# Kernel tuning notes

Hardware: AMD Instinct MI355X
Metric: run time of the kernel (lower is better)

## Reference

```python
import jax, jax.numpy as jnp
import numpy as np

N, B, D = 4, 256, 128  # agents, batch, latent dim; hidden = 2*D


def setup_inputs() -> dict:
    key = jax.random.key(0)
    k1, k2, k3, k4, k5 = jax.random.split(key, 5)
    z_all = jax.random.normal(k1, (N, B, D), dtype=jnp.float32)
    # per-agent MLP params, stacked over agents; torch Linear layout [out, in]
    W1 = jax.random.normal(k2, (N, 2 * D, D), dtype=jnp.float32) * 0.08
    b1 = jax.random.normal(k3, (N, 2 * D), dtype=jnp.float32) * 0.05
    W2 = jax.random.normal(k4, (N, 1, 2 * D), dtype=jnp.float32) * 0.06
    b2 = jax.random.normal(k5, (N, 1), dtype=jnp.float32) * 0.05
    return {"z_all": z_all, "W1": W1, "b1": b1, "W2": W2, "b2": b2}


def _value(z, W1i, b1i, W2i, b2i):
    # V_i(z): Linear(D,2D) -> tanh -> Linear(2D,1), squeezed to scalar
    h = jnp.tanh(W1i @ z + b1i)          # [2D]
    return jnp.dot(W2i[0], h) + b2i[0]   # scalar


def _pair_hessian(zb, W1i, b1i, W2i, b2i):
    # Hessian of V_i w.r.t. z, batched over B -> [B, D, D]
    hess = jax.hessian(lambda z: _value(z, W1i, b1i, W2i, b2i))
    return jax.vmap(hess)(zb)


def reference(z_all, W1, b1, W2, b2):
    Bn, Dn = z_all.shape[1], z_all.shape[2]
    zero = jnp.zeros((Bn, Dn, Dn), dtype=z_all.dtype)
    rows = []
    for i in range(N):
        cols = []
        for j in range(N):
            if i == j:
                cols.append(zero)
            else:
                cols.append(_pair_hessian(z_all[j], W1[i], b1[i], W2[i], b2[i]))
        rows.append(jnp.stack(cols, axis=0))
    return jnp.stack(rows, axis=0)  # [N, N, B, D, D]
```

## Files before the change

### kernel.cpp

```cpp
#include <hip/hip_runtime.h>
#include <hip/hip_bf16.h>

#define NA 4
#define BB 256
#define DDm 128
#define KKm 256

typedef __attribute__((ext_vector_type(4))) float f32x4;
typedef __attribute__((ext_vector_type(4))) unsigned int u32x4;
typedef __attribute__((ext_vector_type(8))) short bf16x8;

__device__ __forceinline__ unsigned int f2bf(float f) {
  unsigned int bits = __builtin_bit_cast(unsigned int, f);
  unsigned int lsb = (bits >> 16) & 1u;
  return (bits + 0x7fffu + lsb) >> 16;
}

__device__ __forceinline__ int swz_off(int a, int k2bytes) {
  return ((a << 9) + k2bytes) ^ ((a & 7) << 4);
}

__global__ __launch_bounds__(256) void prep_kernel(const float* __restrict__ W1,
                                                   unsigned short* __restrict__ Wt_g,
                                                   float* __restrict__ W1T) {
  int blk = blockIdx.x;
  int i = blk >> 3;
  int chunk = blk & 7;
  const float* W1i = W1 + i * KKm * DDm;
  char* Wti = (char*)(Wt_g + i * 32768);
  float* W1Ti = W1T + i * DDm * KKm;
  int base = chunk * 4096;
  for (int idx = base + threadIdx.x; idx < base + 4096; idx += 256) {
    int a = idx >> 8;
    int k = idx & 255;
    float v = W1i[k * DDm + a];
    W1Ti[a * KKm + k] = v;
    *(unsigned short*)(Wti + swz_off(a, k << 1)) = (unsigned short)f2bf(v);
  }
}

__global__ __launch_bounds__(256, 2) void hess_kernel(
    const float* __restrict__ z_all, const float* __restrict__ b1,
    const float* __restrict__ W2, const unsigned short* __restrict__ Wt_g,
    const float* __restrict__ W1T, float* __restrict__ out) {
  __shared__ __align__(16) unsigned short Wt[32768];
  __shared__ __align__(16) float s_lds[2][KKm];

  int t = threadIdx.x;
  int blk = blockIdx.x;
  int pair = blk >> 7;
  int bgrp = blk & 127;
  int i = pair >> 2;
  int j = pair & 3;

  if (i == j) {
    f32x4* zp = (f32x4*)(out + (((size_t)pair * BB + bgrp * 2) << 14));
    f32x4 z4 = (f32x4){0.f, 0.f, 0.f, 0.f};
#pragma unroll
    for (int q = 0; q < 32; ++q) zp[q * 256 + t] = z4;
    return;
  }

  {
    int wvi = t >> 6, lane = t & 63;
    const char* src = (const char*)(Wt_g + i * 32768);
#pragma unroll
    for (int it = 0; it < 16; ++it) {
      int off = (it * 4 + wvi) * 1024;
      __builtin_amdgcn_global_load_lds(
          (const __attribute__((address_space(1))) unsigned int*)(src + off + lane * 16),
          (__attribute__((address_space(3))) unsigned int*)((char*)Wt + off),
          16, 0, 0);
    }
  }

  {
    const float* w = W1T + i * DDm * KKm + t;
    const float* zj = z_all + ((size_t)j * BB + bgrp * 2) * DDm;
    float u0 = b1[i * KKm + t];
    float u1 = u0;
#pragma unroll 8
    for (int a = 0; a < DDm; ++a) {
      float wa = w[a * KKm];
      u0 = fmaf(wa, zj[a], u0);
      u1 = fmaf(wa, zj[DDm + a], u1);
    }
    float w2v = W2[i * KKm + t];
    float h0 = tanhf(u0), h1 = tanhf(u1);
    s_lds[0][t] = -2.0f * w2v * h0 * (1.0f - h0 * h0);
    s_lds[1][t] = -2.0f * w2v * h1 * (1.0f - h1 * h1);
  }
  __syncthreads();

  int wvi = t >> 6, lane = t & 63;
  int bl = wvi >> 1;
  int m0 = (wvi & 1) * 64;
  int g = lane >> 4;
  int lr = lane & 15;

  f32x4 acc[4][8];
#pragma unroll
  for (int mt = 0; mt < 4; ++mt)
#pragma unroll
    for (int nt = 0; nt < 8; ++nt) acc[mt][nt] = (f32x4){0.f, 0.f, 0.f, 0.f};

  for (int kc = 0; kc < 8; ++kc) {
    int kbyte = kc * 64 + g * 16;
    const f32x4* sp = (const f32x4*)&s_lds[bl][kc * 32 + g * 8];
    f32x4 sA = sp[0], sB = sp[1];
    float sv[8] = {sA[0], sA[1], sA[2], sA[3], sB[0], sB[1], sB[2], sB[3]};

    bf16x8 afr[4];
#pragma unroll
    for (int mt = 0; mt < 4; ++mt) {
      int row = m0 + mt * 16 + lr;
      u32x4 wq = *(const u32x4*)((const char*)Wt + swz_off(row, kbyte));
      u32x4 aq;
#pragma unroll
      for (int q = 0; q < 4; ++q) {
        float lo = __builtin_bit_cast(float, wq[q] << 16) * sv[2 * q];
        float hi = __builtin_bit_cast(float, wq[q] & 0xffff0000u) * sv[2 * q + 1];
        aq[q] = f2bf(lo) | (f2bf(hi) << 16);
      }
      afr[mt] = __builtin_bit_cast(bf16x8, aq);
    }

#pragma unroll
    for (int nt = 0; nt < 8; ++nt) {
      int row = nt * 16 + lr;
      bf16x8 bfr = __builtin_bit_cast(
          bf16x8, *(const u32x4*)((const char*)Wt + swz_off(row, kbyte)));
#pragma unroll
      for (int mt = 0; mt < 4; ++mt)
        acc[mt][nt] =
            __builtin_amdgcn_mfma_f32_16x16x32_bf16(afr[mt], bfr, acc[mt][nt], 0, 0, 0);
    }
  }

  int b = bgrp * 2 + bl;
  float* op = out + (((size_t)pair * BB + b) << 14);
#pragma unroll
  for (int mt = 0; mt < 4; ++mt) {
    int rbase = m0 + mt * 16 + g * 4;
#pragma unroll
    for (int nt = 0; nt < 8; ++nt) {
      int col = nt * 16 + lr;
#pragma unroll
      for (int q = 0; q < 4; ++q) op[(size_t)(rbase + q) * DDm + col] = acc[mt][nt][q];
    }
  }
}

extern "C" void kernel_launch(void* const* d_in, const int* in_sizes, int n_in,
                              void* d_out, int out_size, void* d_ws, size_t ws_size,
                              hipStream_t stream) {
  const float* z_all = (const float*)d_in[0];
  const float* W1 = (const float*)d_in[1];
  const float* b1 = (const float*)d_in[2];
  const float* W2 = (const float*)d_in[3];
  float* out = (float*)d_out;

  unsigned short* Wt_g = (unsigned short*)d_ws;
  float* W1T = (float*)((char*)d_ws + 262144);

  prep_kernel<<<32, 256, 0, stream>>>(W1, Wt_g, W1T);
  hess_kernel<<<16 * 128, 256, 0, stream>>>(z_all, b1, W2, Wt_g, W1T, out);
}
```

Measured before the change: 73.77 us.

## Hoist first-layer activations into separate kernel and use hardware bf16 pack

Moves the per-sample hidden pre-activation and tanh computation out of the Hessian kernel into a new kernel. Each thread there computes 16 batch samples, so every W1T column load is reused across 16 samples instead of 2, and the results go to a workspace buffer. The Hessian kernel now just loads the precomputed scale vectors. It also replaces the software float-to-bf16 rounding with the v_cvt_pk_bf16_f32 instruction. The cost is an extra kernel launch and a global round trip for the scale vectors.

After: 87.28 us. 18.3% more time.

```diff
diff --git a/kernel.cpp b/kernel.cpp
--- a/kernel.cpp
+++ b/kernel.cpp
@@ -39,10 +39,40 @@
   }
 }
 
+__global__ __launch_bounds__(256) void sval_kernel(const float* __restrict__ z_all,
+                                                   const float* __restrict__ b1,
+                                                   const float* __restrict__ W2,
+                                                   const float* __restrict__ W1T,
+                                                   float* __restrict__ s_all) {
+  int blk = blockIdx.x;
+  int i = blk >> 6;
+  int j = (blk >> 4) & 3;
+  int bc = blk & 15;
+  if (i == j) return;
+  int t = threadIdx.x;
+  const float* w = W1T + i * DDm * KKm + t;
+  const float* z = z_all + ((size_t)j * BB + bc * 16) * DDm;
+  float u[16];
+  float ub = b1[i * KKm + t];
+#pragma unroll
+  for (int v = 0; v < 16; ++v) u[v] = ub;
+  for (int a = 0; a < DDm; ++a) {
+    float wa = w[a * KKm];
+#pragma unroll
+    for (int v = 0; v < 16; ++v) u[v] = fmaf(wa, z[v * DDm + a], u[v]);
+  }
+  float w2v = W2[i * KKm + t];
+  float* sp = s_all + (((size_t)(i * NA + j) * BB) + bc * 16) * KKm + t;
+#pragma unroll
+  for (int v = 0; v < 16; ++v) {
+    float h = tanhf(u[v]);
+    sp[(size_t)v * KKm] = -2.0f * w2v * h * (1.0f - h * h);
+  }
+}
+
 __global__ __launch_bounds__(256, 2) void hess_kernel(
-    const float* __restrict__ z_all, const float* __restrict__ b1,
-    const float* __restrict__ W2, const unsigned short* __restrict__ Wt_g,
-    const float* __restrict__ W1T, float* __restrict__ out) {
+    const unsigned short* __restrict__ Wt_g, const float* __restrict__ s_all,
+    float* __restrict__ out) {
   __shared__ __align__(16) unsigned short Wt[32768];
   __shared__ __align__(16) float s_lds[2][KKm];
 
@@ -75,20 +105,9 @@
   }
 
   {
-    const float* w = W1T + i * DDm * KKm + t;
-    const float* zj = z_all + ((size_t)j * BB + bgrp * 2) * DDm;
-    float u0 = b1[i * KKm + t];
-    float u1 = u0;
-#pragma unroll 8
-    for (int a = 0; a < DDm; ++a) {
-      float wa = w[a * KKm];
-      u0 = fmaf(wa, zj[a], u0);
-      u1 = fmaf(wa, zj[DDm + a], u1);
-    }
-    float w2v = W2[i * KKm + t];
-    float h0 = tanhf(u0), h1 = tanhf(u1);
-    s_lds[0][t] = -2.0f * w2v * h0 * (1.0f - h0 * h0);
-    s_lds[1][t] = -2.0f * w2v * h1 * (1.0f - h1 * h1);
+    const float* sg = s_all + ((size_t)pair * BB + bgrp * 2) * KKm;
+    s_lds[0][t] = sg[t];
+    s_lds[1][t] = sg[KKm + t];
   }
   __syncthreads();
 
@@ -120,7 +139,9 @@
       for (int q = 0; q < 4; ++q) {
         float lo = __builtin_bit_cast(float, wq[q] << 16) * sv[2 * q];
         float hi = __builtin_bit_cast(float, wq[q] & 0xffff0000u) * sv[2 * q + 1];
-        aq[q] = f2bf(lo) | (f2bf(hi) << 16);
+        unsigned int r;
+        asm("v_cvt_pk_bf16_f32 %0, %1, %2" : "=v"(r) : "v"(lo), "v"(hi));
+        aq[q] = r;
       }
       afr[mt] = __builtin_bit_cast(bf16x8, aq);
     }
@@ -162,7 +183,9 @@
 
   unsigned short* Wt_g = (unsigned short*)d_ws;
   float* W1T = (float*)((char*)d_ws + 262144);
+  float* s_all = (float*)((char*)d_ws + 786432);
 
   prep_kernel<<<32, 256, 0, stream>>>(W1, Wt_g, W1T);
-  hess_kernel<<<16 * 128, 256, 0, stream>>>(z_all, b1, W2, Wt_g, W1T, out);
+  sval_kernel<<<256, 256, 0, stream>>>(z_all, b1, W2, W1T, s_all);
+  hess_kernel<<<16 * 128, 256, 0, stream>>>(Wt_g, s_all, out);
 }
```

## Stage accumulator tiles through LDS for 16-byte coalesced output stores

Applied to the files above, without the earlier changes.

The output epilogue now writes MFMA accumulator tiles into a swizzled LDS staging buffer, reusing the weight tile area after a barrier, and reads them back as contiguous 16-byte vectors. The goal is to replace scattered 4-byte global stores with wide coalesced stores on this write-bound kernel. The manual bf16 rounding is also replaced by the compiler's __bf16 conversion, which may map to a hardware convert instruction. The exchange costs an extra barrier plus LDS write and read traffic per tile, and there is no barrier between reuses of the double-buffered staging slots within a wave.

After: 75.44 us. 1.02x slower.

```diff
diff --git a/kernel.cpp b/kernel.cpp
--- a/kernel.cpp
+++ b/kernel.cpp
@@ -62,11 +62,11 @@
   }
 
   {
-    int wvi = t >> 6, lane = t & 63;
+    int wv = t >> 6, lane = t & 63;
     const char* src = (const char*)(Wt_g + i * 32768);
 #pragma unroll
     for (int it = 0; it < 16; ++it) {
-      int off = (it * 4 + wvi) * 1024;
+      int off = (it * 4 + wv) * 1024;
       __builtin_amdgcn_global_load_lds(
           (const __attribute__((address_space(1))) unsigned int*)(src + off + lane * 16),
           (__attribute__((address_space(3))) unsigned int*)((char*)Wt + off),
@@ -120,7 +120,9 @@
       for (int q = 0; q < 4; ++q) {
         float lo = __builtin_bit_cast(float, wq[q] << 16) * sv[2 * q];
         float hi = __builtin_bit_cast(float, wq[q] & 0xffff0000u) * sv[2 * q + 1];
-        aq[q] = f2bf(lo) | (f2bf(hi) << 16);
+        unsigned int lb = __builtin_bit_cast(unsigned short, (__bf16)lo);
+        unsigned int hb = __builtin_bit_cast(unsigned short, (__bf16)hi);
+        aq[q] = lb | (hb << 16);
       }
       afr[mt] = __builtin_bit_cast(bf16x8, aq);
     }
@@ -137,16 +139,28 @@
     }
   }
 
+  __syncthreads();
+  char* stg = (char*)Wt + wvi * 16384;
   int b = bgrp * 2 + bl;
-  float* op = out + (((size_t)pair * BB + b) << 14);
+  float* op = out + (((size_t)pair * BB + b) << 14) + (size_t)m0 * DDm;
 #pragma unroll
   for (int mt = 0; mt < 4; ++mt) {
-    int rbase = m0 + mt * 16 + g * 4;
+    char* buf = stg + (mt & 1) * 8192;
 #pragma unroll
-    for (int nt = 0; nt < 8; ++nt) {
-      int col = nt * 16 + lr;
+    for (int nt = 0; nt < 8; ++nt)
 #pragma unroll
-      for (int q = 0; q < 4; ++q) op[(size_t)(rbase + q) * DDm + col] = acc[mt][nt][q];
+      for (int q = 0; q < 4; ++q) {
+        int row = g * 4 + q;
+        int el = row * 128 + nt * 16 + lr;
+        int byte = (el * 4) ^ ((row & 12) << 4);
+        *(float*)(buf + byte) = acc[mt][nt][q];
+      }
+#pragma unroll
+    for (int r2 = 0; r2 < 8; ++r2) {
+      int o = r2 * 1024 + lane * 16;
+      int byte = o ^ (((o >> 11) & 3) << 6);
+      f32x4 v = *(const f32x4*)(buf + byte);
+      *(f32x4*)(op + mt * (16 * DDm) + (o >> 2)) = v;
     }
   }
 }
```

## Pre-pack W1 into MFMA fragment order and read it directly from global

Applied to the files above, without the earlier changes.

The prep kernel now writes the bf16 W1 transpose in an MFMA-fragment-major layout, so each lane's 16-byte fragment loads straight from global/L2 and the 64KB LDS staging of W1 per block goes away. Each block now handles one batch element instead of two, doubling the grid, and occupancy is raised to 4 blocks per CU with a smaller accumulator tile. The bf16 rounding uses the native __bf16 conversion. This trades LDS traffic for repeated global (L2-cached) fragment reads, and since the A and B fragments are no longer shared across two batch elements, weight reads per output roughly double.

Result: slower. 103.9 us (+40.8%).

```diff
diff --git a/kernel.cpp b/kernel.cpp
--- a/kernel.cpp
+++ b/kernel.cpp
@@ -16,18 +16,14 @@
   return (bits + 0x7fffu + lsb) >> 16;
 }
 
-__device__ __forceinline__ int swz_off(int a, int k2bytes) {
-  return ((a << 9) + k2bytes) ^ ((a & 7) << 4);
-}
-
 __global__ __launch_bounds__(256) void prep_kernel(const float* __restrict__ W1,
-                                                   unsigned short* __restrict__ Wt_g,
+                                                   unsigned short* __restrict__ Wf_g,
                                                    float* __restrict__ W1T) {
   int blk = blockIdx.x;
   int i = blk >> 3;
   int chunk = blk & 7;
   const float* W1i = W1 + i * KKm * DDm;
-  char* Wti = (char*)(Wt_g + i * 32768);
+  char* Wfi = (char*)(Wf_g + i * 32768);
   float* W1Ti = W1T + i * DDm * KKm;
   int base = chunk * 4096;
   for (int idx = base + threadIdx.x; idx < base + 4096; idx += 256) {
@@ -35,118 +31,101 @@
     int k = idx & 255;
     float v = W1i[k * DDm + a];
     W1Ti[a * KKm + k] = v;
-    *(unsigned short*)(Wti + swz_off(a, k << 1)) = (unsigned short)f2bf(v);
+    int kc = k >> 5, g = (k >> 3) & 3, ke = k & 7, rb = a >> 4, lr = a & 15;
+    size_t off = (size_t)(((kc * 8 + rb) * 64 + lr * 4 + g) * 16 + ke * 2);
+    *(unsigned short*)(Wfi + off) = (unsigned short)f2bf(v);
   }
 }
 
-__global__ __launch_bounds__(256, 2) void hess_kernel(
+__global__ __launch_bounds__(256, 4) void hess_kernel(
     const float* __restrict__ z_all, const float* __restrict__ b1,
-    const float* __restrict__ W2, const unsigned short* __restrict__ Wt_g,
+    const float* __restrict__ W2, const unsigned short* __restrict__ Wf_g,
     const float* __restrict__ W1T, float* __restrict__ out) {
-  __shared__ __align__(16) unsigned short Wt[32768];
-  __shared__ __align__(16) float s_lds[2][KKm];
+  __shared__ float s_lds[KKm];
 
   int t = threadIdx.x;
   int blk = blockIdx.x;
-  int pair = blk >> 7;
-  int bgrp = blk & 127;
+  int pair = blk >> 8;
+  int b = blk & 255;
   int i = pair >> 2;
   int j = pair & 3;
+  float* op0 = out + (((size_t)pair * BB + b) << 14);
 
   if (i == j) {
-    f32x4* zp = (f32x4*)(out + (((size_t)pair * BB + bgrp * 2) << 14));
     f32x4 z4 = (f32x4){0.f, 0.f, 0.f, 0.f};
+    f32x4* zp = (f32x4*)op0;
 #pragma unroll
-    for (int q = 0; q < 32; ++q) zp[q * 256 + t] = z4;
+    for (int q = 0; q < 16; ++q) zp[q * 256 + t] = z4;
     return;
   }
 
   {
-    int wvi = t >> 6, lane = t & 63;
-    const char* src = (const char*)(Wt_g + i * 32768);
-#pragma unroll
-    for (int it = 0; it < 16; ++it) {
-      int off = (it * 4 + wvi) * 1024;
-      __builtin_amdgcn_global_load_lds(
-          (const __attribute__((address_space(1))) unsigned int*)(src + off + lane * 16),
-          (__attribute__((address_space(3))) unsigned int*)((char*)Wt + off),
-          16, 0, 0);
-    }
-  }
-
-  {
     const float* w = W1T + i * DDm * KKm + t;
-    const float* zj = z_all + ((size_t)j * BB + bgrp * 2) * DDm;
-    float u0 = b1[i * KKm + t];
-    float u1 = u0;
+    const float* zj = z_all + ((size_t)j * BB + b) * DDm;
+    float u = b1[i * KKm + t];
 #pragma unroll 8
-    for (int a = 0; a < DDm; ++a) {
-      float wa = w[a * KKm];
-      u0 = fmaf(wa, zj[a], u0);
-      u1 = fmaf(wa, zj[DDm + a], u1);
-    }
+    for (int a = 0; a < DDm; ++a) u = fmaf(w[a * KKm], zj[a], u);
     float w2v = W2[i * KKm + t];
-    float h0 = tanhf(u0), h1 = tanhf(u1);
-    s_lds[0][t] = -2.0f * w2v * h0 * (1.0f - h0 * h0);
-    s_lds[1][t] = -2.0f * w2v * h1 * (1.0f - h1 * h1);
+    float h = tanhf(u);
+    s_lds[t] = -2.0f * w2v * h * (1.0f - h * h);
   }
   __syncthreads();
 
   int wvi = t >> 6, lane = t & 63;
-  int bl = wvi >> 1;
-  int m0 = (wvi & 1) * 64;
   int g = lane >> 4;
   int lr = lane & 15;
+  int m0 = wvi * 32;
 
-  f32x4 acc[4][8];
+  f32x4 acc[2][8];
 #pragma unroll
-  for (int mt = 0; mt < 4; ++mt)
+  for (int mt = 0; mt < 2; ++mt)
 #pragma unroll
     for (int nt = 0; nt < 8; ++nt) acc[mt][nt] = (f32x4){0.f, 0.f, 0.f, 0.f};
 
+  const char* wf = (const char*)(Wf_g + i * 32768) + (lr * 4 + g) * 16;
+
   for (int kc = 0; kc < 8; ++kc) {
-    int kbyte = kc * 64 + g * 16;
-    const f32x4* sp = (const f32x4*)&s_lds[bl][kc * 32 + g * 8];
+    const char* base = wf + kc * 8192;
+    const char* abase = base + wvi * 2048;
+    u32x4 a0 = *(const u32x4*)abase;
+    u32x4 a1 = *(const u32x4*)(abase + 1024);
+
+    const f32x4* sp = (const f32x4*)&s_lds[kc * 32 + g * 8];
     f32x4 sA = sp[0], sB = sp[1];
     float sv[8] = {sA[0], sA[1], sA[2], sA[3], sB[0], sB[1], sB[2], sB[3]};
 
-    bf16x8 afr[4];
+    bf16x8 afr[2];
 #pragma unroll
-    for (int mt = 0; mt < 4; ++mt) {
-      int row = m0 + mt * 16 + lr;
-      u32x4 wq = *(const u32x4*)((const char*)Wt + swz_off(row, kbyte));
+    for (int mt = 0; mt < 2; ++mt) {
+      u32x4 wq = mt ? a1 : a0;
       u32x4 aq;
 #pragma unroll
       for (int q = 0; q < 4; ++q) {
         float lo = __builtin_bit_cast(float, wq[q] << 16) * sv[2 * q];
         float hi = __builtin_bit_cast(float, wq[q] & 0xffff0000u) * sv[2 * q + 1];
-        aq[q] = f2bf(lo) | (f2bf(hi) << 16);
+        unsigned int lb = __builtin_bit_cast(unsigned short, (__bf16)lo);
+        unsigned int hb = __builtin_bit_cast(unsigned short, (__bf16)hi);
+        aq[q] = lb | (hb << 16);
       }
       afr[mt] = __builtin_bit_cast(bf16x8, aq);
     }
 
 #pragma unroll
     for (int nt = 0; nt < 8; ++nt) {
-      int row = nt * 16 + lr;
-      bf16x8 bfr = __builtin_bit_cast(
-          bf16x8, *(const u32x4*)((const char*)Wt + swz_off(row, kbyte)));
-#pragma unroll
-      for (int mt = 0; mt < 4; ++mt)
-        acc[mt][nt] =
-            __builtin_amdgcn_mfma_f32_16x16x32_bf16(afr[mt], bfr, acc[mt][nt], 0, 0, 0);
+      bf16x8 bfr = *(const bf16x8*)(base + nt * 1024);
+      acc[0][nt] = __builtin_amdgcn_mfma_f32_16x16x32_bf16(afr[0], bfr, acc[0][nt], 0, 0, 0);
+      acc[1][nt] = __builtin_amdgcn_mfma_f32_16x16x32_bf16(afr[1], bfr, acc[1][nt], 0, 0, 0);
     }
   }
 
-  int b = bgrp * 2 + bl;
-  float* op = out + (((size_t)pair * BB + b) << 14);
 #pragma unroll
-  for (int mt = 0; mt < 4; ++mt) {
+  for (int mt = 0; mt < 2; ++mt) {
     int rbase = m0 + mt * 16 + g * 4;
 #pragma unroll
     for (int nt = 0; nt < 8; ++nt) {
       int col = nt * 16 + lr;
 #pragma unroll
-      for (int q = 0; q < 4; ++q) op[(size_t)(rbase + q) * DDm + col] = acc[mt][nt][q];
+      for (int q = 0; q < 4; ++q) op0[(size_t)(rbase + q) * DDm + col] = acc[mt][nt][q];
     }
   }
 }
@@ -160,9 +139,9 @@
   const float* W2 = (const float*)d_in[3];
   float* out = (float*)d_out;
 
-  unsigned short* Wt_g = (unsigned short*)d_ws;
+  unsigned short* Wf_g = (unsigned short*)d_ws;
   float* W1T = (float*)((char*)d_ws + 262144);
 
-  prep_kernel<<<32, 256, 0, stream>>>(W1, Wt_g, W1T);
-  hess_kernel<<<16 * 128, 256, 0, stream>>>(z_all, b1, W2, Wt_g, W1T, out);
+  prep_kernel<<<32, 256, 0, stream>>>(W1, Wf_g, W1T);
+  hess_kernel<<<16 * 256, 256, 0, stream>>>(z_all, b1, W2, Wf_g, W1T, out);
 }
```
